# Performance work log

Hardware: AMD Instinct MI355X
Metric: run time of the kernel (lower is better)

Reference implementation:

```python
import jax, jax.numpy as jnp
import numpy as np

NUM_HEADS = 12
DIM = 768
HEAD_DIM = DIM // NUM_HEADS
NUM_BUCKETS = 32
MAX_DISTANCE = 128
ELEV_SCALE = 1000.0


def _bucket_positions(relative_position):
    # Faithful port of RelativePositionBias2D._bucket_positions (torch .long() truncates;
    # values passed through the large branch are non-negative so astype(int32) matches).
    nb = NUM_BUCKETS // 2  # 16
    n = -relative_position
    ret = (n < 0).astype(jnp.int32) * nb
    n = jnp.abs(n)
    max_exact = nb // 2  # 8
    is_small = n < max_exact
    n_safe = jnp.maximum(n, 1).astype(jnp.float32)  # avoid log(0); masked by is_small
    val_if_large = max_exact + (
        jnp.log(n_safe / max_exact) / np.float32(np.log(MAX_DISTANCE / max_exact)) * (nb - max_exact)
    ).astype(jnp.int32)
    val_if_large = jnp.minimum(val_if_large, nb - 1)
    return ret + jnp.where(is_small, n, val_if_large)


def _bucket_idx(coords_2d):
    # coords_2d: [B, N, 2] in [0,1] -> integer grid coords
    coords_int = (coords_2d * MAX_DISTANCE).astype(jnp.int32)
    rel_x = coords_int[:, :, None, 0] - coords_int[:, None, :, 0]  # [B,N,N]
    rel_y = coords_int[:, :, None, 1] - coords_int[:, None, :, 1]
    bx = _bucket_positions(rel_x)
    by = _bucket_positions(rel_y)
    return bx * NUM_BUCKETS + by  # [B,N,N] int32 in [0, 1024)


def setup_inputs() -> dict:
    key = jax.random.key(0)
    ks = jax.random.split(key, 8)
    B, N, D = 4, 1024, DIM
    x = jax.random.normal(ks[0], (B, N, D), dtype=jnp.float32)
    coords_2d = jax.random.uniform(ks[1], (B, N, 2), dtype=jnp.float32)
    elevation_patches = jax.random.normal(ks[2], (B, N), dtype=jnp.float32) * 2000.0  # meters
    qkv_w = jax.random.normal(ks[3], (3 * D, D), dtype=jnp.float32) * 0.02
    qkv_b = jnp.zeros((3 * D,), dtype=jnp.float32)
    proj_w = jax.random.normal(ks[4], (D, D), dtype=jnp.float32) * 0.02
    proj_b = jnp.zeros((D,), dtype=jnp.float32)
    bias_table = jax.random.normal(ks[5], (NUM_BUCKETS * NUM_BUCKETS, NUM_HEADS), dtype=jnp.float32) * 0.02
    alpha = jnp.full((1,), 2.0, dtype=jnp.float32)
    return {"x": x, "coords_2d": coords_2d, "elevation_patches": elevation_patches,
            "qkv_w": qkv_w, "qkv_b": qkv_b, "proj_w": proj_w, "proj_b": proj_b,
            "bias_table": bias_table, "alpha": alpha}


def reference(x, coords_2d, elevation_patches, qkv_w, qkv_b, proj_w, proj_b, bias_table, alpha):
    B, N, D = x.shape
    H, hd = NUM_HEADS, HEAD_DIM
    scale = hd ** -0.5

    qkv = x @ qkv_w.T + qkv_b  # [B,N,3D]
    qkv = qkv.reshape(B, N, 3, H, hd)
    q = qkv[:, :, 0].transpose(0, 2, 1, 3)  # [B,H,N,hd]
    k = qkv[:, :, 1].transpose(0, 2, 1, 3)
    v = qkv[:, :, 2].transpose(0, 2, 1, 3)

    attn = jnp.einsum('bhnd,bhmd->bhnm', q * scale, k)  # [B,H,N,N]

    # relative position bias: gather from table, [B,N,N,H] -> [B,H,N,N]
    idx = _bucket_idx(coords_2d)
    rel_bias = bias_table[idx].transpose(0, 3, 1, 2)
    attn = attn + rel_bias

    # elevation bias: [B,N,N], broadcast over heads
    elev_diff = (elevation_patches[:, None, :] - elevation_patches[:, :, None]) / ELEV_SCALE
    elev_bias = jnp.clip(-alpha[0] * jax.nn.relu(elev_diff), -10.0, 0.0)
    attn = attn + elev_bias[:, None, :, :]

    attn = jax.nn.softmax(attn.astype(jnp.float32), axis=-1).astype(q.dtype)

    out = jnp.einsum('bhnm,bhmd->bhnd', attn, v)  # [B,H,N,hd]
    out = out.transpose(0, 2, 1, 3).reshape(B, N, D)
    return out @ proj_w.T + proj_b
```

## Files before the change

### kernel.cpp

```cpp
#include <hip/hip_runtime.h>
#include <hip/hip_bf16.h>
#include <math.h>

#define NH 12
#define HD 64
#define NSEQ 1024
#define DMODEL 768
#define LOG2E 1.44269504f

typedef unsigned short ushort_t;
typedef float f32x4 __attribute__((ext_vector_type(4)));
typedef short bf16x8 __attribute__((ext_vector_type(8)));

__device__ __forceinline__ ushort_t f2bf(float f) {
    unsigned int u = __float_as_uint(f);
    u += 0x7FFFu + ((u >> 16) & 1u);
    return (ushort_t)(u >> 16);
}

__device__ __forceinline__ unsigned pk2(float x, float y) {
    __hip_bfloat162 t = __float22bfloat162_rn(make_float2(x, y));
    union { __hip_bfloat162 b; unsigned u; } c; c.b = t;
    return c.u;
}

#define XB_N   3145728u
#define WQB_N  1769472u
#define PWB_N  589824u
#define CVT_BLOCKS 2688

__device__ __forceinline__ int bucketf(int rel) {
    const int n = -rel;
    const int u = (n < 0) ? 16 : 0;
    const int a = n < 0 ? -n : n;
    if (a < 8) return u + a;
    int v = 8 + (int)(log2f((float)a * 0.125f) * 2.0f + 1e-4f);
    if (v > 15) v = 15;
    return u + v;
}

__global__ __launch_bounds__(256) void prep_kernel(
    const float* __restrict__ x, const float* __restrict__ w1,
    const float* __restrict__ w2, ushort_t* __restrict__ dst,
    const float* __restrict__ coords, const float* __restrict__ elev,
    const float* __restrict__ alpha_p, unsigned* __restrict__ pack)
{
    const int t = threadIdx.x;
    if (blockIdx.x < CVT_BLOCKS) {
        const unsigned i = blockIdx.x * 256 + t;
        const unsigned n0 = XB_N / 8, n1 = n0 + WQB_N / 8, n2 = n1 + PWB_N / 8;
        if (i >= n2) return;
        const float* src; unsigned off;
        if (i < n0)      { src = x;  off = i; }
        else if (i < n1) { src = w1; off = i - n0; }
        else             { src = w2; off = i - n1; }
        const float4 a = ((const float4*)src)[off * 2];
        const float4 b = ((const float4*)src)[off * 2 + 1];
        uint4 pk;
        pk.x = pk2(a.x, a.y); pk.y = pk2(a.z, a.w);
        pk.z = pk2(b.x, b.y); pk.w = pk2(b.z, b.w);
        ((uint4*)dst)[i] = pk;
    } else {
        const int blk = blockIdx.x - CVT_BLOCKS;
        const int b = blk >> 10, i = blk & 1023;
        const float alpha = alpha_p[0];
        const float2 ci = *(const float2*)&coords[(size_t)(b * NSEQ + i) * 2];
        const int cxi = (int)(ci.x * 128.0f), cyi = (int)(ci.y * 128.0f);
        const float ei = elev[b * NSEQ + i];
        const int j0 = t * 4;
        const float4 c01 = *(const float4*)&coords[(size_t)(b * NSEQ + j0) * 2];
        const float4 c23 = *(const float4*)&coords[(size_t)(b * NSEQ + j0 + 2) * 2];
        const float4 ej4 = *(const float4*)&elev[b * NSEQ + j0];
        const float cjx[4] = {c01.x, c01.z, c23.x, c23.z};
        const float cjy[4] = {c01.y, c01.w, c23.y, c23.w};
        const float ejv[4] = {ej4.x, ej4.y, ej4.z, ej4.w};
        unsigned r[4];
        #pragma unroll
        for (int k = 0; k < 4; ++k) {
            const int bx = bucketf(cxi - (int)(cjx[k] * 128.0f));
            const int by = bucketf(cyi - (int)(cjy[k] * 128.0f));
            const int idx = (bx << 5) + by;
            const float ed = (ejv[k] - ei) * 1e-3f;
            const float eb = fmaxf(-alpha * fmaxf(ed, 0.0f), -10.0f) * LOG2E;
            r[k] = ((unsigned)f2bf(eb) << 16) | (unsigned)idx;
        }
        uint4 o; o.x = r[0]; o.y = r[1]; o.z = r[2]; o.w = r[3];
        *(uint4*)&pack[((size_t)b << 20) + (size_t)i * NSEQ + j0] = o;
    }
}

__global__ __launch_bounds__(256) void qkv_gemm(
    const ushort_t* __restrict__ A, const ushort_t* __restrict__ B,
    const float* __restrict__ bias,
    ushort_t* __restrict__ Qb, ushort_t* __restrict__ Kb, ushort_t* __restrict__ Vtb)
{
    __shared__ __align__(16) ushort_t As[128 * 40];
    __shared__ __align__(16) ushort_t Bs[128 * 40];
    const int t = threadIdx.x;
    const int lane = t & 63, w = t >> 6;
    const int wr = w >> 1, wc = w & 1;
    const int col = lane & 15, quad = lane >> 4;
    const int m0 = blockIdx.y * 128, c0 = blockIdx.x * 128;

    const f32x4 zero = {0.f, 0.f, 0.f, 0.f};
    f32x4 acc[4][4];
    #pragma unroll
    for (int i = 0; i < 4; ++i)
        #pragma unroll
        for (int j = 0; j < 4; ++j) acc[i][j] = zero;

    const int row_s = t >> 2, cq = (t & 3) * 8;
    for (int k0 = 0; k0 < DMODEL; k0 += 32) {
        const uint4 a0 = *(const uint4*)&A[(size_t)(m0 + row_s) * DMODEL + k0 + cq];
        const uint4 a1 = *(const uint4*)&A[(size_t)(m0 + 64 + row_s) * DMODEL + k0 + cq];
        const uint4 b0 = *(const uint4*)&B[(size_t)(c0 + row_s) * DMODEL + k0 + cq];
        const uint4 b1 = *(const uint4*)&B[(size_t)(c0 + 64 + row_s) * DMODEL + k0 + cq];
        __syncthreads();
        *(uint4*)&As[row_s * 40 + cq] = a0;
        *(uint4*)&As[(64 + row_s) * 40 + cq] = a1;
        *(uint4*)&Bs[row_s * 40 + cq] = b0;
        *(uint4*)&Bs[(64 + row_s) * 40 + cq] = b1;
        __syncthreads();
        bf16x8 af[4], bf[4];
        #pragma unroll
        for (int im = 0; im < 4; ++im)
            af[im] = *(const bf16x8*)&As[(wr * 64 + im * 16 + col) * 40 + quad * 8];
        #pragma unroll
        for (int jn = 0; jn < 4; ++jn)
            bf[jn] = *(const bf16x8*)&Bs[(wc * 64 + jn * 16 + col) * 40 + quad * 8];
        #pragma unroll
        for (int im = 0; im < 4; ++im)
            #pragma unroll
            for (int jn = 0; jn < 4; ++jn)
                acc[im][jn] = __builtin_amdgcn_mfma_f32_16x16x32_bf16(af[im], bf[jn], acc[im][jn], 0, 0, 0);
    }

    const int cb = c0 + wc * 64;
    const int s = cb / DMODEL;
    const int h = (cb % DMODEL) >> 6;
    const int b = m0 >> 10;
    const int bh = b * NH + h;
    const int n0 = (m0 & (NSEQ - 1)) + wr * 64;
    const float qsc = 0.125f * LOG2E;

    #pragma unroll
    for (int im = 0; im < 4; ++im) {
        #pragma unroll
        for (int jn = 0; jn < 4; ++jn) {
            const int d = jn * 16 + col;
            const float bv = bias[cb + d];
            const f32x4 a = acc[im][jn];
            if (s == 0) {
                #pragma unroll
                for (int r = 0; r < 4; ++r) {
                    const int n = n0 + im * 16 + quad * 4 + r;
                    Qb[((size_t)bh * NSEQ + n) * HD + d] = f2bf((a[r] + bv) * qsc);
                }
            } else if (s == 1) {
                #pragma unroll
                for (int r = 0; r < 4; ++r) {
                    const int n = n0 + im * 16 + quad * 4 + r;
                    Kb[((size_t)bh * NSEQ + n) * HD + d] = f2bf(a[r] + bv);
                }
            } else {
                uint2 p;
                p.x = pk2(a[0] + bv, a[1] + bv);
                p.y = pk2(a[2] + bv, a[3] + bv);
                *(uint2*)&Vtb[((size_t)bh * HD + d) * NSEQ + n0 + im * 16 + quad * 4] = p;
            }
        }
    }
}

__global__ __launch_bounds__(256) void attn_mfma(
    const ushort_t* __restrict__ Qb, const ushort_t* __restrict__ Kb,
    const ushort_t* __restrict__ Vtb,
    const unsigned* __restrict__ pack,
    const float* __restrict__ table,
    ushort_t* __restrict__ Ob)
{
    __shared__ __align__(16) ushort_t Ks[2][64 * 72];
    __shared__ __align__(16) ushort_t Vt[2][64 * 72];
    __shared__ __align__(16) ushort_t Ps[64 * 72];
    __shared__ float tab[1024];
    __shared__ float red[4];

    const int t = threadIdx.x;
    const int lane = t & 63, w = t >> 6;
    const int col = lane & 15, quad = lane >> 4;
    const int bid = blockIdx.x;
    const int it = bid & 15, bh = bid >> 4;
    const int h = bh % NH, b = bh / NH;
    const int i0 = it * 64;

    float lm = -1e30f;
    for (int i = t; i < 1024; i += 256) {
        const float v = table[i * NH + h] * LOG2E;
        tab[i] = v;
        lm = fmaxf(lm, v);
    }
    #pragma unroll
    for (int off = 1; off < 64; off <<= 1)
        lm = fmaxf(lm, __shfl_xor(lm, off));
    if (lane == 0) red[w] = lm;

    const ushort_t* Qg = Qb + ((size_t)bh * NSEQ + i0 + w * 16 + col) * HD;
    const bf16x8 aq0 = *(const bf16x8*)(Qg + quad * 8);
    const bf16x8 aq1 = *(const bf16x8*)(Qg + 32 + quad * 8);

    const size_t kvbase = (size_t)bh * NSEQ * HD;
    const unsigned* prow = pack + ((size_t)b << 20)
                         + (size_t)(i0 + w * 16 + col) * NSEQ + quad * 4;

    const int srow = t >> 3, sc8 = (t & 7) * 8;
    const int so0 = srow * 72 + sc8;
    const int so1 = (srow + 32) * 72 + sc8;

    uint4 k0 = *(const uint4*)&Kb[kvbase + (size_t)srow * HD + sc8];
    uint4 k1 = *(const uint4*)&Kb[kvbase + (size_t)(srow + 32) * HD + sc8];
    uint4 v0 = *(const uint4*)&Vtb[kvbase + (size_t)srow * NSEQ + sc8];
    uint4 v1 = *(const uint4*)&Vtb[kvbase + (size_t)(srow + 32) * NSEQ + sc8];
    *(uint4*)&Ks[0][so0] = k0;
    *(uint4*)&Ks[0][so1] = k1;
    *(uint4*)&Vt[0][so0] = v0;
    *(uint4*)&Vt[0][so1] = v1;
    k0 = *(const uint4*)&Kb[kvbase + (size_t)(64 + srow) * HD + sc8];
    k1 = *(const uint4*)&Kb[kvbase + (size_t)(64 + srow + 32) * HD + sc8];
    v0 = *(const uint4*)&Vtb[kvbase + (size_t)srow * NSEQ + 64 + sc8];
    v1 = *(const uint4*)&Vtb[kvbase + (size_t)(srow + 32) * NSEQ + 64 + sc8];

    const f32x4 zero = {0.f, 0.f, 0.f, 0.f};
    f32x4 o_acc[4];
    #pragma unroll
    for (int i = 0; i < 4; ++i) o_acc[i] = zero;
    float m_l = -1e30f;
    float l_l = 0.f;
    float maxrb = 0.f;

    #pragma unroll 2
    for (int jt = 0; jt < 16; ++jt) {
        __syncthreads();
        if (jt == 0) maxrb = fmaxf(fmaxf(red[0], red[1]), fmaxf(red[2], red[3]));
        const int cur = jt & 1;
        const int j0 = jt * 64;

        if (jt < 15) {
            *(uint4*)&Ks[cur ^ 1][so0] = k0;
            *(uint4*)&Ks[cur ^ 1][so1] = k1;
            *(uint4*)&Vt[cur ^ 1][so0] = v0;
            *(uint4*)&Vt[cur ^ 1][so1] = v1;
        }
        if (jt < 14) {
            const int j2 = (jt + 2) * 64;
            k0 = *(const uint4*)&Kb[kvbase + (size_t)(j2 + srow) * HD + sc8];
            k1 = *(const uint4*)&Kb[kvbase + (size_t)(j2 + srow + 32) * HD + sc8];
            v0 = *(const uint4*)&Vtb[kvbase + (size_t)srow * NSEQ + j2 + sc8];
            v1 = *(const uint4*)&Vtb[kvbase + (size_t)(srow + 32) * NSEQ + j2 + sc8];
        }
        uint4 pk4[4];
        #pragma unroll
        for (int jb = 0; jb < 4; ++jb)
            pk4[jb] = *(const uint4*)(prow + j0 + jb * 16);

        f32x4 sacc[4];
        #pragma unroll
        for (int jb = 0; jb < 4; ++jb) {
            sacc[jb] = zero;
            const bf16x8 kb0 = *(const bf16x8*)&Ks[cur][(jb * 16 + col) * 72 + quad * 8];
            const bf16x8 kb1 = *(const bf16x8*)&Ks[cur][(jb * 16 + col) * 72 + 32 + quad * 8];
            sacc[jb] = __builtin_amdgcn_mfma_f32_16x16x32_bf16(kb0, aq0, sacc[jb], 0, 0, 0);
            sacc[jb] = __builtin_amdgcn_mfma_f32_16x16x32_bf16(kb1, aq1, sacc[jb], 0, 0, 0);
        }

        float mx = fmaxf(fmaxf(fmaxf(sacc[0][0], sacc[0][1]), fmaxf(sacc[0][2], sacc[0][3])),
                         fmaxf(fmaxf(sacc[1][0], sacc[1][1]), fmaxf(sacc[1][2], sacc[1][3])));
        mx = fmaxf(mx, fmaxf(fmaxf(fmaxf(sacc[2][0], sacc[2][1]), fmaxf(sacc[2][2], sacc[2][3])),
                             fmaxf(fmaxf(sacc[3][0], sacc[3][1]), fmaxf(sacc[3][2], sacc[3][3]))));
        mx = fmaxf(mx, __shfl_xor(mx, 16));
        mx = fmaxf(mx, __shfl_xor(mx, 32));
        const float m_new = fmaxf(m_l, mx + maxrb);
        const float corr = exp2f(m_l - m_new);
        m_l = m_new;

        float psum = 0.f;
        #pragma unroll
        for (int jb = 0; jb < 4; ++jb) {
            const uint4 pkv = pk4[jb];
            const float p0 = exp2f(sacc[jb][0] + tab[pkv.x & 1023u] + __uint_as_float(pkv.x & 0xFFFF0000u) - m_new);
            const float p1 = exp2f(sacc[jb][1] + tab[pkv.y & 1023u] + __uint_as_float(pkv.y & 0xFFFF0000u) - m_new);
            const float p2 = exp2f(sacc[jb][2] + tab[pkv.z & 1023u] + __uint_as_float(pkv.z & 0xFFFF0000u) - m_new);
            const float p3 = exp2f(sacc[jb][3] + tab[pkv.w & 1023u] + __uint_as_float(pkv.w & 0xFFFF0000u) - m_new);
            psum += (p0 + p1) + (p2 + p3);
            uint2 st;
            st.x = pk2(p0, p1);
            st.y = pk2(p2, p3);
            *(uint2*)&Ps[(w * 16 + col) * 72 + jb * 16 + quad * 4] = st;
        }
        l_l = l_l * corr + psum;

        float corr_r[4];
        #pragma unroll
        for (int r = 0; r < 4; ++r)
            corr_r[r] = __shfl(corr, w * 16 + quad * 4 + r);
        #pragma unroll
        for (int db = 0; db < 4; ++db) {
            o_acc[db][0] *= corr_r[0]; o_acc[db][1] *= corr_r[1];
            o_acc[db][2] *= corr_r[2]; o_acc[db][3] *= corr_r[3];
        }

        const bf16x8 ap0 = *(const bf16x8*)&Ps[(w * 16 + col) * 72 + quad * 8];
        const bf16x8 ap1 = *(const bf16x8*)&Ps[(w * 16 + col) * 72 + 32 + quad * 8];
        #pragma unroll
        for (int db = 0; db < 4; ++db) {
            const bf16x8 vv0 = *(const bf16x8*)&Vt[cur][(db * 16 + col) * 72 + quad * 8];
            const bf16x8 vv1 = *(const bf16x8*)&Vt[cur][(db * 16 + col) * 72 + 32 + quad * 8];
            o_acc[db] = __builtin_amdgcn_mfma_f32_16x16x32_bf16(ap0, vv0, o_acc[db], 0, 0, 0);
            o_acc[db] = __builtin_amdgcn_mfma_f32_16x16x32_bf16(ap1, vv1, o_acc[db], 0, 0, 0);
        }
    }

    float l = l_l;
    l += __shfl_xor(l, 16);
    l += __shfl_xor(l, 32);
    #pragma unroll
    for (int r = 0; r < 4; ++r) {
        const float lr = __shfl(l, w * 16 + quad * 4 + r);
        const float inv = 1.f / lr;
        const int ri = w * 16 + quad * 4 + r;
        const size_t base = ((size_t)(b * NSEQ) + i0 + ri) * DMODEL + h * HD;
        #pragma unroll
        for (int db = 0; db < 4; ++db)
            Ob[base + db * 16 + col] = f2bf(o_acc[db][r] * inv);
    }
}

__global__ __launch_bounds__(256) void proj_gemm(
    const ushort_t* __restrict__ A, const ushort_t* __restrict__ B,
    const float* __restrict__ bias, float* __restrict__ out)
{
    __shared__ __align__(16) ushort_t As[64 * 40];
    __shared__ __align__(16) ushort_t Bs[64 * 40];
    const int t = threadIdx.x;
    const int lane = t & 63, w = t >> 6;
    const int wr = w >> 1, wc = w & 1;
    const int col = lane & 15, quad = lane >> 4;
    const int m0 = blockIdx.y * 64, c0 = blockIdx.x * 64;

    const f32x4 zero = {0.f, 0.f, 0.f, 0.f};
    f32x4 acc[2][2];
    #pragma unroll
    for (int i = 0; i < 2; ++i)
        #pragma unroll
        for (int j = 0; j < 2; ++j) acc[i][j] = zero;

    const int srow = t >> 2, sc8 = (t & 3) * 8;
    for (int k0 = 0; k0 < DMODEL; k0 += 32) {
        const uint4 a0 = *(const uint4*)&A[(size_t)(m0 + srow) * DMODEL + k0 + sc8];
        const uint4 b0 = *(const uint4*)&B[(size_t)(c0 + srow) * DMODEL + k0 + sc8];
        __syncthreads();
        *(uint4*)&As[srow * 40 + sc8] = a0;
        *(uint4*)&Bs[srow * 40 + sc8] = b0;
        __syncthreads();
        bf16x8 af[2], bf[2];
        #pragma unroll
        for (int im = 0; im < 2; ++im)
            af[im] = *(const bf16x8*)&As[(wr * 32 + im * 16 + col) * 40 + quad * 8];
        #pragma unroll
        for (int jn = 0; jn < 2; ++jn)
            bf[jn] = *(const bf16x8*)&Bs[(wc * 32 + jn * 16 + col) * 40 + quad * 8];
        #pragma unroll
        for (int im = 0; im < 2; ++im)
            #pragma unroll
            for (int jn = 0; jn < 2; ++jn)
                acc[im][jn] = __builtin_amdgcn_mfma_f32_16x16x32_bf16(af[im], bf[jn], acc[im][jn], 0, 0, 0);
    }

    #pragma unroll
    for (int im = 0; im < 2; ++im) {
        #pragma unroll
        for (int jn = 0; jn < 2; ++jn) {
            const int c = c0 + wc * 32 + jn * 16 + col;
            const float bv = bias[c];
            #pragma unroll
            for (int r = 0; r < 4; ++r) {
                const int m = m0 + wr * 32 + im * 16 + quad * 4 + r;
                out[(size_t)m * DMODEL + c] = acc[im][jn][r] + bv;
            }
        }
    }
}

extern "C" void kernel_launch(void* const* d_in, const int* in_sizes, int n_in,
                              void* d_out, int out_size, void* d_ws, size_t ws_size,
                              hipStream_t stream) {
    const float* x       = (const float*)d_in[0];
    const float* coords  = (const float*)d_in[1];
    const float* elev    = (const float*)d_in[2];
    const float* qkv_w   = (const float*)d_in[3];
    const float* qkv_b   = (const float*)d_in[4];
    const float* proj_w  = (const float*)d_in[5];
    const float* proj_b  = (const float*)d_in[6];
    const float* btable  = (const float*)d_in[7];
    const float* alpha   = (const float*)d_in[8];
    float* out = (float*)d_out;

    ushort_t* wsu = (ushort_t*)d_ws;
    ushort_t* xb  = wsu;
    ushort_t* wqb = wsu + 3145728;
    ushort_t* pwb = wsu + 4915200;
    ushort_t* Qb  = wsu + 5505024;
    ushort_t* Kb  = wsu + 8650752;
    ushort_t* Vtb = wsu + 11796480;
    ushort_t* Ob  = wsu + 14942208;
    unsigned* pck = (unsigned*)(wsu + 18087936);

    prep_kernel<<<CVT_BLOCKS + 4096, 256, 0, stream>>>(
        x, qkv_w, proj_w, wsu, coords, elev, alpha, pck);
    qkv_gemm<<<dim3(18, 32), 256, 0, stream>>>(xb, wqb, qkv_b, Qb, Kb, Vtb);
    attn_mfma<<<768, 256, 0, stream>>>(Qb, Kb, Vtb, pck, btable, Ob);
    proj_gemm<<<dim3(12, 64), 256, 0, stream>>>(Ob, pwb, proj_b, out);
}
```

Before: 194.2 us.

## Double-buffer QKV and proj GEMM tiles, prefetch bias pack, skip redundant rescale

The QKV GEMM and projection GEMM now use double-buffered shared-memory tiles with register prefetch two steps ahead, so each K step needs one barrier instead of two and global loads overlap the MFMAs. The projection GEMM also widens its K step to 96 per stage. The attention kernel prefetches the packed bias/index words one tile ahead and skips rescaling the output accumulator when no row's running max grew. This costs more LDS and registers, which may lower occupancy.

```diff
diff --git a/kernel.cpp b/kernel.cpp
--- a/kernel.cpp
+++ b/kernel.cpp
@@ -94,8 +94,8 @@
     const float* __restrict__ bias,
     ushort_t* __restrict__ Qb, ushort_t* __restrict__ Kb, ushort_t* __restrict__ Vtb)
 {
-    __shared__ __align__(16) ushort_t As[128 * 40];
-    __shared__ __align__(16) ushort_t Bs[128 * 40];
+    __shared__ __align__(16) ushort_t As[2][128 * 40];
+    __shared__ __align__(16) ushort_t Bs[2][128 * 40];
     const int t = threadIdx.x;
     const int lane = t & 63, w = t >> 6;
     const int wr = w >> 1, wc = w & 1;
@@ -110,24 +110,50 @@
         for (int j = 0; j < 4; ++j) acc[i][j] = zero;
 
     const int row_s = t >> 2, cq = (t & 3) * 8;
-    for (int k0 = 0; k0 < DMODEL; k0 += 32) {
-        const uint4 a0 = *(const uint4*)&A[(size_t)(m0 + row_s) * DMODEL + k0 + cq];
-        const uint4 a1 = *(const uint4*)&A[(size_t)(m0 + 64 + row_s) * DMODEL + k0 + cq];
-        const uint4 b0 = *(const uint4*)&B[(size_t)(c0 + row_s) * DMODEL + k0 + cq];
-        const uint4 b1 = *(const uint4*)&B[(size_t)(c0 + 64 + row_s) * DMODEL + k0 + cq];
+    const int so = row_s * 40 + cq;
+    const ushort_t* Ag = A + (size_t)(m0 + row_s) * DMODEL + cq;
+    const ushort_t* Bg = B + (size_t)(c0 + row_s) * DMODEL + cq;
+    const size_t h64 = (size_t)64 * DMODEL;
+
+    {
+        const uint4 x0 = *(const uint4*)(Ag);
+        const uint4 x1 = *(const uint4*)(Ag + h64);
+        const uint4 y0 = *(const uint4*)(Bg);
+        const uint4 y1 = *(const uint4*)(Bg + h64);
+        *(uint4*)&As[0][so] = x0;
+        *(uint4*)&As[0][so + 64 * 40] = x1;
+        *(uint4*)&Bs[0][so] = y0;
+        *(uint4*)&Bs[0][so + 64 * 40] = y1;
+    }
+    uint4 pa0 = *(const uint4*)(Ag + 32);
+    uint4 pa1 = *(const uint4*)(Ag + h64 + 32);
+    uint4 pb0 = *(const uint4*)(Bg + 32);
+    uint4 pb1 = *(const uint4*)(Bg + h64 + 32);
+
+    #pragma unroll 2
+    for (int ks = 0; ks < 24; ++ks) {
         __syncthreads();
-        *(uint4*)&As[row_s * 40 + cq] = a0;
-        *(uint4*)&As[(64 + row_s) * 40 + cq] = a1;
-        *(uint4*)&Bs[row_s * 40 + cq] = b0;
-        *(uint4*)&Bs[(64 + row_s) * 40 + cq] = b1;
-        __syncthreads();
+        const int cur = ks & 1;
+        if (ks < 23) {
+            *(uint4*)&As[cur ^ 1][so] = pa0;
+            *(uint4*)&As[cur ^ 1][so + 64 * 40] = pa1;
+            *(uint4*)&Bs[cur ^ 1][so] = pb0;
+            *(uint4*)&Bs[cur ^ 1][so + 64 * 40] = pb1;
+        }
+        if (ks < 22) {
+            const int k2 = (ks + 2) * 32;
+            pa0 = *(const uint4*)(Ag + k2);
+            pa1 = *(const uint4*)(Ag + h64 + k2);
+            pb0 = *(const uint4*)(Bg + k2);
+            pb1 = *(const uint4*)(Bg + h64 + k2);
+        }
         bf16x8 af[4], bf[4];
         #pragma unroll
         for (int im = 0; im < 4; ++im)
-            af[im] = *(const bf16x8*)&As[(wr * 64 + im * 16 + col) * 40 + quad * 8];
+            af[im] = *(const bf16x8*)&As[cur][(wr * 64 + im * 16 + col) * 40 + quad * 8];
         #pragma unroll
         for (int jn = 0; jn < 4; ++jn)
-            bf[jn] = *(const bf16x8*)&Bs[(wc * 64 + jn * 16 + col) * 40 + quad * 8];
+            bf[jn] = *(const bf16x8*)&Bs[cur][(wc * 64 + jn * 16 + col) * 40 + quad * 8];
         #pragma unroll
         for (int im = 0; im < 4; ++im)
             #pragma unroll
@@ -229,6 +255,11 @@
     v0 = *(const uint4*)&Vtb[kvbase + (size_t)srow * NSEQ + 64 + sc8];
     v1 = *(const uint4*)&Vtb[kvbase + (size_t)(srow + 32) * NSEQ + 64 + sc8];
 
+    uint4 pk4[2][4];
+    #pragma unroll
+    for (int jb = 0; jb < 4; ++jb)
+        pk4[0][jb] = *(const uint4*)(prow + jb * 16);
+
     const f32x4 zero = {0.f, 0.f, 0.f, 0.f};
     f32x4 o_acc[4];
     #pragma unroll
@@ -242,7 +273,6 @@
         __syncthreads();
         if (jt == 0) maxrb = fmaxf(fmaxf(red[0], red[1]), fmaxf(red[2], red[3]));
         const int cur = jt & 1;
-        const int j0 = jt * 64;
 
         if (jt < 15) {
             *(uint4*)&Ks[cur ^ 1][so0] = k0;
@@ -257,10 +287,12 @@
             v0 = *(const uint4*)&Vtb[kvbase + (size_t)srow * NSEQ + j2 + sc8];
             v1 = *(const uint4*)&Vtb[kvbase + (size_t)(srow + 32) * NSEQ + j2 + sc8];
         }
-        uint4 pk4[4];
-        #pragma unroll
-        for (int jb = 0; jb < 4; ++jb)
-            pk4[jb] = *(const uint4*)(prow + j0 + jb * 16);
+        if (jt < 15) {
+            const int j1 = (jt + 1) * 64;
+            #pragma unroll
+            for (int jb = 0; jb < 4; ++jb)
+                pk4[cur ^ 1][jb] = *(const uint4*)(prow + j1 + jb * 16);
+        }
 
         f32x4 sacc[4];
         #pragma unroll
@@ -278,14 +310,16 @@
                              fmaxf(fmaxf(sacc[3][0], sacc[3][1]), fmaxf(sacc[3][2], sacc[3][3]))));
         mx = fmaxf(mx, __shfl_xor(mx, 16));
         mx = fmaxf(mx, __shfl_xor(mx, 32));
-        const float m_new = fmaxf(m_l, mx + maxrb);
-        const float corr = exp2f(m_l - m_new);
+        const float m_old = m_l;
+        const float m_new = fmaxf(m_old, mx + maxrb);
+        const bool grew = m_new > m_old;
+        const float corr = grew ? exp2f(m_old - m_new) : 1.0f;
         m_l = m_new;
 
         float psum = 0.f;
         #pragma unroll
         for (int jb = 0; jb < 4; ++jb) {
-            const uint4 pkv = pk4[jb];
+            const uint4 pkv = pk4[cur][jb];
             const float p0 = exp2f(sacc[jb][0] + tab[pkv.x & 1023u] + __uint_as_float(pkv.x & 0xFFFF0000u) - m_new);
             const float p1 = exp2f(sacc[jb][1] + tab[pkv.y & 1023u] + __uint_as_float(pkv.y & 0xFFFF0000u) - m_new);
             const float p2 = exp2f(sacc[jb][2] + tab[pkv.z & 1023u] + __uint_as_float(pkv.z & 0xFFFF0000u) - m_new);
@@ -298,14 +332,16 @@
         }
         l_l = l_l * corr + psum;
 
-        float corr_r[4];
-        #pragma unroll
-        for (int r = 0; r < 4; ++r)
-            corr_r[r] = __shfl(corr, w * 16 + quad * 4 + r);
-        #pragma unroll
-        for (int db = 0; db < 4; ++db) {
-            o_acc[db][0] *= corr_r[0]; o_acc[db][1] *= corr_r[1];
-            o_acc[db][2] *= corr_r[2]; o_acc[db][3] *= corr_r[3];
+        if (__any(grew)) {
+            float corr_r[4];
+            #pragma unroll
+            for (int r = 0; r < 4; ++r)
+                corr_r[r] = __shfl(corr, w * 16 + quad * 4 + r);
+            #pragma unroll
+            for (int db = 0; db < 4; ++db) {
+                o_acc[db][0] *= corr_r[0]; o_acc[db][1] *= corr_r[1];
+                o_acc[db][2] *= corr_r[2]; o_acc[db][3] *= corr_r[3];
+            }
         }
 
         const bf16x8 ap0 = *(const bf16x8*)&Ps[(w * 16 + col) * 72 + quad * 8];
@@ -338,8 +374,8 @@
     const ushort_t* __restrict__ A, const ushort_t* __restrict__ B,
     const float* __restrict__ bias, float* __restrict__ out)
 {
-    __shared__ __align__(16) ushort_t As[64 * 40];
-    __shared__ __align__(16) ushort_t Bs[64 * 40];
+    __shared__ __align__(16) ushort_t As[2][64 * 104];
+    __shared__ __align__(16) ushort_t Bs[2][64 * 104];
     const int t = threadIdx.x;
     const int lane = t & 63, w = t >> 6;
     const int wr = w >> 1, wc = w & 1;
@@ -354,25 +390,58 @@
         for (int j = 0; j < 2; ++j) acc[i][j] = zero;
 
     const int srow = t >> 2, sc8 = (t & 3) * 8;
-    for (int k0 = 0; k0 < DMODEL; k0 += 32) {
-        const uint4 a0 = *(const uint4*)&A[(size_t)(m0 + srow) * DMODEL + k0 + sc8];
-        const uint4 b0 = *(const uint4*)&B[(size_t)(c0 + srow) * DMODEL + k0 + sc8];
+    const int so = srow * 104 + sc8;
+    const ushort_t* Ag = A + (size_t)(m0 + srow) * DMODEL + sc8;
+    const ushort_t* Bg = B + (size_t)(c0 + srow) * DMODEL + sc8;
+
+    {
+        #pragma unroll
+        for (int c = 0; c < 3; ++c) {
+            *(uint4*)&As[0][so + c * 32] = *(const uint4*)(Ag + c * 32);
+            *(uint4*)&Bs[0][so + c * 32] = *(const uint4*)(Bg + c * 32);
+        }
+    }
+    uint4 pa[3], pb[3];
+    #pragma unroll
+    for (int c = 0; c < 3; ++c) {
+        pa[c] = *(const uint4*)(Ag + 96 + c * 32);
+        pb[c] = *(const uint4*)(Bg + 96 + c * 32);
+    }
+
+    #pragma unroll 2
+    for (int ks = 0; ks < 8; ++ks) {
         __syncthreads();
-        *(uint4*)&As[srow * 40 + sc8] = a0;
-        *(uint4*)&Bs[srow * 40 + sc8] = b0;
-        __syncthreads();
-        bf16x8 af[2], bf[2];
-        #pragma unroll
-        for (int im = 0; im < 2; ++im)
-            af[im] = *(const bf16x8*)&As[(wr * 32 + im * 16 + col) * 40 + quad * 8];
-        #pragma unroll
-        for (int jn = 0; jn < 2; ++jn)
-            bf[jn] = *(const bf16x8*)&Bs[(wc * 32 + jn * 16 + col) * 40 + quad * 8];
-        #pragma unroll
-        for (int im = 0; im < 2; ++im)
+        const int cur = ks & 1;
+        if (ks < 7) {
+            #pragma unroll
+            for (int c = 0; c < 3; ++c) {
+                *(uint4*)&As[cur ^ 1][so + c * 32] = pa[c];
+                *(uint4*)&Bs[cur ^ 1][so + c * 32] = pb[c];
+            }
+        }
+        if (ks < 6) {
+            const int k2 = (ks + 2) * 96;
+            #pragma unroll
+            for (int c = 0; c < 3; ++c) {
+                pa[c] = *(const uint4*)(Ag + k2 + c * 32);
+                pb[c] = *(const uint4*)(Bg + k2 + c * 32);
+            }
+        }
+        #pragma unroll
+        for (int kc = 0; kc < 3; ++kc) {
+            bf16x8 af[2], bf[2];
+            #pragma unroll
+            for (int im = 0; im < 2; ++im)
+                af[im] = *(const bf16x8*)&As[cur][(wr * 32 + im * 16 + col) * 104 + kc * 32 + quad * 8];
             #pragma unroll
             for (int jn = 0; jn < 2; ++jn)
-                acc[im][jn] = __builtin_amdgcn_mfma_f32_16x16x32_bf16(af[im], bf[jn], acc[im][jn], 0, 0, 0);
+                bf[jn] = *(const bf16x8*)&Bs[cur][(wc * 32 + jn * 16 + col) * 104 + kc * 32 + quad * 8];
+            #pragma unroll
+            for (int im = 0; im < 2; ++im)
+                #pragma unroll
+                for (int jn = 0; jn < 2; ++jn)
+                    acc[im][jn] = __builtin_amdgcn_mfma_f32_16x16x32_bf16(af[im], bf[jn], acc[im][jn], 0, 0, 0);
+        }
     }
 
     #pragma unroll
```

New measurement: 219.2 us. +12.9%, slower.
